# Performance work log

Hardware: AMD Instinct MI355X
Metric: run time of the kernel (lower is better)

Reference implementation:

```python
import jax, jax.numpy as jnp
import numpy as np

B, OUT, IN = 1024, 512, 1024

def setup_inputs() -> dict:
    key = jax.random.key(0)
    k1, k2, k3, k4 = jax.random.split(key, 4)
    x = jax.random.uniform(k1, (B, IN), dtype=jnp.float32)            # inputs in [0,1]
    w = jax.random.uniform(k2, (OUT, IN), dtype=jnp.float32)          # centers in [min_input, max_input]=[0,1]
    u = jax.random.uniform(k3, (OUT, IN), dtype=jnp.float32, minval=0.2, maxval=0.7)  # slopes per init
    andor01 = jax.random.randint(k4, (1, OUT), 0, 2).astype(jnp.float32)  # frozen 0/1 mix ('*' mode)
    return {"x": x, "w": w, "u": u, "andor01": andor01}

def reference(x, w, u, andor01):
    # xuw = u * (x[b,None,i] - w[o,i]) ; z[b,o] = sum_i xuw^2 ; y = exp(-z)
    diff = u[None, :, :] * (x[:, None, :] - w[None, :, :])   # [B, OUT, IN]
    z = jnp.sum(diff * diff, axis=-1)                        # [B, OUT]
    y = jnp.exp(-z)                                          # forward of LargeAttractorExp
    # andor == '*': y + andor01 * (1 - 2y)
    return y + andor01 * (1.0 - 2.0 * y)
```

## Files before the change

kernel.cpp:

```cpp
#include <hip/hip_runtime.h>

#define B_SZ   1024
#define OUT_SZ 512
#define IN_SZ  1024

#define MB 64
#define NB 64
#define KSPLIT 4
#define KSL (IN_SZ / KSPLIT)
#define CH  64
#define NCH (KSL / CH)

typedef __bf16 bf16x8 __attribute__((ext_vector_type(8)));
typedef __bf16 bf16x4 __attribute__((ext_vector_type(4)));
typedef float  f32x4  __attribute__((ext_vector_type(4)));

#define A_IDX(seg, s, mf, slot) (((((seg)*2 + (s))*4 + (mf))*64 + (slot))*8)
#define B_IDX(seg, s, nf, slot) (((((seg)*2 + (s))*4 + (nf))*64 + (slot))*8)

__global__ __launch_bounds__(256) void rbf_fused(
    const float* __restrict__ x, const float* __restrict__ w,
    const float* __restrict__ u, float* __restrict__ part)
{
    __shared__ __bf16 Asm[2 * 2 * 4 * 64 * 8];
    __shared__ __bf16 Bsm[3 * 2 * 4 * 64 * 8];

    const int t     = threadIdx.x;
    const int lane  = t & 63;
    const int wv    = t >> 6;
    const int wm    = wv >> 1;
    const int wn    = wv & 1;
    const int mBase = blockIdx.x * MB;
    const int nBase = blockIdx.y * NB;
    const int kz    = blockIdx.z;
    const int kBase = kz * KSL;

    f32x4 acc[2][2] = {};
    f32x4 acc_r[2]  = {};

    bf16x8 ones;
    #pragma unroll
    for (int j = 0; j < 8; ++j) ones[j] = (__bf16)1.f;

    float4 xr[4], ur[4], wr[4];

    auto load_regs = [&](int c) {
        #pragma unroll
        for (int i = 0; i < 4; ++i) {
            int id  = i * 256 + t;
            int row = id >> 4;
            int gk  = kBase + c * CH + (id & 15) * 4;
            xr[i] = *(const float4*)&x[(size_t)(mBase + row) * IN_SZ + gk];
            ur[i] = *(const float4*)&u[(size_t)(nBase + row) * IN_SZ + gk];
            wr[i] = *(const float4*)&w[(size_t)(nBase + row) * IN_SZ + gk];
        }
    };

    auto write_lds = [&]() {
        #pragma unroll
        for (int i = 0; i < 4; ++i) {
            int id    = i * 256 + t;
            int row   = id >> 4;
            int row16 = row & 15;
            int frag  = row >> 4;
            int kl    = (id & 15) * 4;
            int s     = kl >> 5;
            int quad  = (kl >> 3) & 3;
            int j0    = kl & 7;
            int slot  = quad * 16 + ((row16 ^ quad) & 15);

            float xv[4] = {xr[i].x, xr[i].y, xr[i].z, xr[i].w};
            float uv[4] = {ur[i].x, ur[i].y, ur[i].z, ur[i].w};
            float wv4[4] = {wr[i].x, wr[i].y, wr[i].z, wr[i].w};
            bf16x4 a0, a1, b0, b1, b2;
            #pragma unroll
            for (int e = 0; e < 4; ++e) {
                float xe = xv[e], ue = uv[e], we = wv4[e];
                float u2 = ue * ue;
                float uw = ue * we;
                a0[e] = (__bf16)(xe * xe);
                a1[e] = (__bf16)xe;
                b0[e] = (__bf16)u2;
                b1[e] = (__bf16)(-2.f * u2 * we);
                b2[e] = (__bf16)(uw * uw);
            }
            *(bf16x4*)&Asm[A_IDX(0, s, frag, slot) + j0] = a0;
            *(bf16x4*)&Asm[A_IDX(1, s, frag, slot) + j0] = a1;
            *(bf16x4*)&Bsm[B_IDX(0, s, frag, slot) + j0] = b0;
            *(bf16x4*)&Bsm[B_IDX(1, s, frag, slot) + j0] = b1;
            *(bf16x4*)&Bsm[B_IDX(2, s, frag, slot) + j0] = b2;
        }
    };

    const int r_quad = lane >> 4;
    const int r_slot = r_quad * 16 + (((lane & 15) ^ r_quad) & 15);
    const int mf0 = wm * 2, nf0 = wn * 2;

    load_regs(0);

    for (int c = 0; c < NCH; ++c) {
        __syncthreads();
        write_lds();
        __syncthreads();
        if (c + 1 < NCH) load_regs(c + 1);

        #pragma unroll
        for (int seg = 0; seg < 2; ++seg)
            #pragma unroll
            for (int s = 0; s < 2; ++s) {
                bf16x8 am0 = *(const bf16x8*)&Asm[A_IDX(seg, s, mf0,     r_slot)];
                bf16x8 am1 = *(const bf16x8*)&Asm[A_IDX(seg, s, mf0 + 1, r_slot)];
                bf16x8 bn0 = *(const bf16x8*)&Bsm[B_IDX(seg, s, nf0,     r_slot)];
                bf16x8 bn1 = *(const bf16x8*)&Bsm[B_IDX(seg, s, nf0 + 1, r_slot)];
                acc[0][0] = __builtin_amdgcn_mfma_f32_16x16x32_bf16(am0, bn0, acc[0][0], 0, 0, 0);
                acc[0][1] = __builtin_amdgcn_mfma_f32_16x16x32_bf16(am0, bn1, acc[0][1], 0, 0, 0);
                acc[1][0] = __builtin_amdgcn_mfma_f32_16x16x32_bf16(am1, bn0, acc[1][0], 0, 0, 0);
                acc[1][1] = __builtin_amdgcn_mfma_f32_16x16x32_bf16(am1, bn1, acc[1][1], 0, 0, 0);
            }
        #pragma unroll
        for (int s = 0; s < 2; ++s) {
            bf16x8 b20 = *(const bf16x8*)&Bsm[B_IDX(2, s, nf0,     r_slot)];
            bf16x8 b21 = *(const bf16x8*)&Bsm[B_IDX(2, s, nf0 + 1, r_slot)];
            acc_r[0] = __builtin_amdgcn_mfma_f32_16x16x32_bf16(ones, b20, acc_r[0], 0, 0, 0);
            acc_r[1] = __builtin_amdgcn_mfma_f32_16x16x32_bf16(ones, b21, acc_r[1], 0, 0, 0);
        }
    }

    const int col = lane & 15;
    #pragma unroll
    for (int mi = 0; mi < 2; ++mi) {
        int b = mBase + (wm * 2 + mi) * 16 + r_quad * 4;
        #pragma unroll
        for (int ni = 0; ni < 2; ++ni) {
            int o = nBase + (wn * 2 + ni) * 16 + col;
            #pragma unroll
            for (int r = 0; r < 4; ++r)
                part[((size_t)kz * B_SZ + (b + r)) * OUT_SZ + o] =
                    acc[mi][ni][r] + acc_r[ni][r];
        }
    }
}

__global__ __launch_bounds__(256) void rbf_reduce(
    const float* __restrict__ part, const float* __restrict__ andor,
    float* __restrict__ out)
{
    int idx = blockIdx.x * 256 + threadIdx.x;
    if (idx < B_SZ * OUT_SZ) {
        float z = 0.f;
        #pragma unroll
        for (int kz = 0; kz < KSPLIT; ++kz)
            z += part[(size_t)kz * (B_SZ * OUT_SZ) + idx];
        float a = andor[idx & (OUT_SZ - 1)];
        float y = __expf(-z);
        out[idx] = fmaf(y, 1.f - 2.f * a, a);
    }
}

extern "C" void kernel_launch(void* const* d_in, const int* in_sizes, int n_in,
                              void* d_out, int out_size, void* d_ws, size_t ws_size,
                              hipStream_t stream) {
    const float* x = (const float*)d_in[0];
    const float* w = (const float*)d_in[1];
    const float* u = (const float*)d_in[2];
    const float* a = (const float*)d_in[3];
    float* out = (float*)d_out;

    float* part = (float*)d_ws;

    dim3 grid(B_SZ / MB, OUT_SZ / NB, KSPLIT);
    rbf_fused<<<grid, dim3(256), 0, stream>>>(x, w, u, part);
    rbf_reduce<<<dim3((B_SZ * OUT_SZ) / 256), dim3(256), 0, stream>>>(part, a, out);
}
```

Measured before the change: 75.32 us.

## Precompute bf16 operand images in a prep kernel and stream them via global-to-LDS loads

```diff
diff --git a/kernel.cpp b/kernel.cpp
--- a/kernel.cpp
+++ b/kernel.cpp
@@ -3,158 +3,184 @@
 #define B_SZ   1024
 #define OUT_SZ 512
 #define IN_SZ  1024
+#define KK     2048
 
 #define MB 64
 #define NB 64
-#define KSPLIT 4
-#define KSL (IN_SZ / KSPLIT)
+#define KSPLIT 8
+#define KSL (KK / KSPLIT)
 #define CH  64
 #define NCH (KSL / CH)
+#define NKC (KK / CH)
+#define CHUNK_ENT 512
 
 typedef __bf16 bf16x8 __attribute__((ext_vector_type(8)));
-typedef __bf16 bf16x4 __attribute__((ext_vector_type(4)));
 typedef float  f32x4  __attribute__((ext_vector_type(4)));
 
-#define A_IDX(seg, s, mf, slot) (((((seg)*2 + (s))*4 + (mf))*64 + (slot))*8)
-#define B_IDX(seg, s, nf, slot) (((((seg)*2 + (s))*4 + (nf))*64 + (slot))*8)
-
-__global__ __launch_bounds__(256) void rbf_fused(
+#define PART_BYTES ((size_t)KSPLIT * B_SZ * OUT_SZ * 4)
+#define AIMG_OFF   PART_BYTES
+#define AIMG_BYTES ((size_t)(B_SZ / MB) * NKC * CHUNK_ENT * 16)
+#define BIMG_OFF   (AIMG_OFF + AIMG_BYTES)
+#define BIMG_BYTES ((size_t)(OUT_SZ / NB) * NKC * CHUNK_ENT * 16)
+#define RB_OFF     (BIMG_OFF + BIMG_BYTES)
+
+__global__ __launch_bounds__(256) void rbf_prep(
     const float* __restrict__ x, const float* __restrict__ w,
-    const float* __restrict__ u, float* __restrict__ part)
+    const float* __restrict__ u, __bf16* __restrict__ Aimg,
+    __bf16* __restrict__ Bimg, float* __restrict__ rbias)
 {
-    __shared__ __bf16 Asm[2 * 2 * 4 * 64 * 8];
-    __shared__ __bf16 Bsm[3 * 2 * 4 * 64 * 8];
-
-    const int t     = threadIdx.x;
-    const int lane  = t & 63;
-    const int wv    = t >> 6;
-    const int wm    = wv >> 1;
-    const int wn    = wv & 1;
-    const int mBase = blockIdx.x * MB;
-    const int nBase = blockIdx.y * NB;
-    const int kz    = blockIdx.z;
-    const int kBase = kz * KSL;
+    const int bid = blockIdx.x, t = threadIdx.x;
+    if (bid < 1024) {
+        const int e    = (bid << 8) + t;
+        const int slot = e & 63;
+        const int frag = (e >> 6) & 3;
+        const int s    = (e >> 8) & 1;
+        const int kc   = (e >> 9) & 31;
+        const int mT   = e >> 14;
+        const int row  = mT * 64 + frag * 16 + (slot & 15);
+        const int k0   = kc * 64 + s * 32 + (slot >> 4) * 8;
+        const float* src = &x[(size_t)row * IN_SZ + (k0 & (IN_SZ - 1))];
+        float4 v0 = *(const float4*)src;
+        float4 v1 = *(const float4*)(src + 4);
+        float vv[8] = {v0.x, v0.y, v0.z, v0.w, v1.x, v1.y, v1.z, v1.w};
+        bf16x8 o8;
+        if (k0 < IN_SZ) {
+            #pragma unroll
+            for (int j = 0; j < 8; ++j) o8[j] = (__bf16)(vv[j] * vv[j]);
+        } else {
+            #pragma unroll
+            for (int j = 0; j < 8; ++j) o8[j] = (__bf16)vv[j];
+        }
+        *(bf16x8*)&Aimg[(size_t)e * 8] = o8;
+    } else if (bid < 1536) {
+        const int e    = ((bid - 1024) << 8) + t;
+        const int slot = e & 63;
+        const int frag = (e >> 6) & 3;
+        const int s    = (e >> 8) & 1;
+        const int kc   = (e >> 9) & 31;
+        const int nT   = e >> 14;
+        const int row  = nT * 64 + frag * 16 + (slot & 15);
+        const int k0   = kc * 64 + s * 32 + (slot >> 4) * 8;
+        const size_t off = (size_t)row * IN_SZ + (k0 & (IN_SZ - 1));
+        float4 u0 = *(const float4*)&u[off];
+        float4 u1 = *(const float4*)&u[off + 4];
+        float uu[8] = {u0.x, u0.y, u0.z, u0.w, u1.x, u1.y, u1.z, u1.w};
+        bf16x8 o8;
+        if (k0 < IN_SZ) {
+            #pragma unroll
+            for (int j = 0; j < 8; ++j) o8[j] = (__bf16)(uu[j] * uu[j]);
+        } else {
+            float4 w0 = *(const float4*)&w[off];
+            float4 w1 = *(const float4*)&w[off + 4];
+            float ww[8] = {w0.x, w0.y, w0.z, w0.w, w1.x, w1.y, w1.z, w1.w};
+            #pragma unroll
+            for (int j = 0; j < 8; ++j) o8[j] = (__bf16)(-2.f * uu[j] * uu[j] * ww[j]);
+        }
+        *(bf16x8*)&Bimg[(size_t)e * 8] = o8;
+    } else {
+        const int o = ((bid - 1536) << 5) + (t >> 3);
+        const size_t base = (size_t)o * IN_SZ + (size_t)(t & 7) * 128;
+        float s = 0.f;
+        for (int k2 = 0; k2 < 128; k2 += 4) {
+            float4 uu = *(const float4*)&u[base + k2];
+            float4 ww = *(const float4*)&w[base + k2];
+            float p0 = uu.x * ww.x, p1 = uu.y * ww.y;
+            float p2 = uu.z * ww.z, p3 = uu.w * ww.w;
+            s = fmaf(p0, p0, s); s = fmaf(p1, p1, s);
+            s = fmaf(p2, p2, s); s = fmaf(p3, p3, s);
+        }
+        s += __shfl_xor(s, 1);
+        s += __shfl_xor(s, 2);
+        s += __shfl_xor(s, 4);
+        if ((t & 7) == 0) rbias[o] = s;
+    }
+}
+
+__device__ __forceinline__ void gld_lds16(const __bf16* g, __bf16* l) {
+    __builtin_amdgcn_global_load_lds(
+        (const __attribute__((address_space(1))) void*)g,
+        (__attribute__((address_space(3))) void*)l, 16, 0, 0);
+}
+
+__global__ __launch_bounds__(256) void rbf_gemm(
+    const __bf16* __restrict__ Aimg, const __bf16* __restrict__ Bimg,
+    float* __restrict__ part)
+{
+    __shared__ __bf16 Asm[2][CHUNK_ENT * 8];
+    __shared__ __bf16 Bsm[2][CHUNK_ENT * 8];
+
+    const int t = threadIdx.x, lane = t & 63;
+    const int wv = t >> 6, wm = wv >> 1, wn = wv & 1;
+    const int mT = blockIdx.x, nT = blockIdx.y, kz = blockIdx.z;
 
     f32x4 acc[2][2] = {};
-    f32x4 acc_r[2]  = {};
-
-    bf16x8 ones;
-    #pragma unroll
-    for (int j = 0; j < 8; ++j) ones[j] = (__bf16)1.f;
-
-    float4 xr[4], ur[4], wr[4];
-
-    auto load_regs = [&](int c) {
-        #pragma unroll
-        for (int i = 0; i < 4; ++i) {
-            int id  = i * 256 + t;
-            int row = id >> 4;
-            int gk  = kBase + c * CH + (id & 15) * 4;
-            xr[i] = *(const float4*)&x[(size_t)(mBase + row) * IN_SZ + gk];
-            ur[i] = *(const float4*)&u[(size_t)(nBase + row) * IN_SZ + gk];
-            wr[i] = *(const float4*)&w[(size_t)(nBase + row) * IN_SZ + gk];
-        }
+
+    const __bf16* gA = &Aimg[(size_t)(mT * NKC + kz * NCH) * CHUNK_ENT * 8];
+    const __bf16* gB = &Bimg[(size_t)(nT * NKC + kz * NCH) * CHUNK_ENT * 8];
+
+    auto stage = [&](int buf, int c) {
+        const __bf16* ga = gA + (size_t)c * CHUNK_ENT * 8;
+        const __bf16* gb = gB + (size_t)c * CHUNK_ENT * 8;
+        gld_lds16(ga + (size_t)t * 8,         &Asm[buf][t * 8]);
+        gld_lds16(ga + (size_t)(t + 256) * 8, &Asm[buf][(t + 256) * 8]);
+        gld_lds16(gb + (size_t)t * 8,         &Bsm[buf][t * 8]);
+        gld_lds16(gb + (size_t)(t + 256) * 8, &Bsm[buf][(t + 256) * 8]);
     };
 
-    auto write_lds = [&]() {
-        #pragma unroll
-        for (int i = 0; i < 4; ++i) {
-            int id    = i * 256 + t;
-            int row   = id >> 4;
-            int row16 = row & 15;
-            int frag  = row >> 4;
-            int kl    = (id & 15) * 4;
-            int s     = kl >> 5;
-            int quad  = (kl >> 3) & 3;
-            int j0    = kl & 7;
-            int slot  = quad * 16 + ((row16 ^ quad) & 15);
-
-            float xv[4] = {xr[i].x, xr[i].y, xr[i].z, xr[i].w};
-            float uv[4] = {ur[i].x, ur[i].y, ur[i].z, ur[i].w};
-            float wv4[4] = {wr[i].x, wr[i].y, wr[i].z, wr[i].w};
-            bf16x4 a0, a1, b0, b1, b2;
-            #pragma unroll
-            for (int e = 0; e < 4; ++e) {
-                float xe = xv[e], ue = uv[e], we = wv4[e];
-                float u2 = ue * ue;
-                float uw = ue * we;
-                a0[e] = (__bf16)(xe * xe);
-                a1[e] = (__bf16)xe;
-                b0[e] = (__bf16)u2;
-                b1[e] = (__bf16)(-2.f * u2 * we);
-                b2[e] = (__bf16)(uw * uw);
-            }
-            *(bf16x4*)&Asm[A_IDX(0, s, frag, slot) + j0] = a0;
-            *(bf16x4*)&Asm[A_IDX(1, s, frag, slot) + j0] = a1;
-            *(bf16x4*)&Bsm[B_IDX(0, s, frag, slot) + j0] = b0;
-            *(bf16x4*)&Bsm[B_IDX(1, s, frag, slot) + j0] = b1;
-            *(bf16x4*)&Bsm[B_IDX(2, s, frag, slot) + j0] = b2;
-        }
-    };
-
-    const int r_quad = lane >> 4;
-    const int r_slot = r_quad * 16 + (((lane & 15) ^ r_quad) & 15);
-    const int mf0 = wm * 2, nf0 = wn * 2;
-
-    load_regs(0);
-
+    stage(0, 0);
+    #pragma unroll
     for (int c = 0; c < NCH; ++c) {
         __syncthreads();
-        write_lds();
-        __syncthreads();
-        if (c + 1 < NCH) load_regs(c + 1);
-
-        #pragma unroll
-        for (int seg = 0; seg < 2; ++seg)
-            #pragma unroll
-            for (int s = 0; s < 2; ++s) {
-                bf16x8 am0 = *(const bf16x8*)&Asm[A_IDX(seg, s, mf0,     r_slot)];
-                bf16x8 am1 = *(const bf16x8*)&Asm[A_IDX(seg, s, mf0 + 1, r_slot)];
-                bf16x8 bn0 = *(const bf16x8*)&Bsm[B_IDX(seg, s, nf0,     r_slot)];
-                bf16x8 bn1 = *(const bf16x8*)&Bsm[B_IDX(seg, s, nf0 + 1, r_slot)];
-                acc[0][0] = __builtin_amdgcn_mfma_f32_16x16x32_bf16(am0, bn0, acc[0][0], 0, 0, 0);
-                acc[0][1] = __builtin_amdgcn_mfma_f32_16x16x32_bf16(am0, bn1, acc[0][1], 0, 0, 0);
-                acc[1][0] = __builtin_amdgcn_mfma_f32_16x16x32_bf16(am1, bn0, acc[1][0], 0, 0, 0);
-                acc[1][1] = __builtin_amdgcn_mfma_f32_16x16x32_bf16(am1, bn1, acc[1][1], 0, 0, 0);
-            }
+        if (c + 1 < NCH) stage((c + 1) & 1, c + 1);
+        const __bf16* Ab = Asm[c & 1];
+        const __bf16* Bb = Bsm[c & 1];
         #pragma unroll
         for (int s = 0; s < 2; ++s) {
-            bf16x8 b20 = *(const bf16x8*)&Bsm[B_IDX(2, s, nf0,     r_slot)];
-            bf16x8 b21 = *(const bf16x8*)&Bsm[B_IDX(2, s, nf0 + 1, r_slot)];
-            acc_r[0] = __builtin_amdgcn_mfma_f32_16x16x32_bf16(ones, b20, acc_r[0], 0, 0, 0);
-            acc_r[1] = __builtin_amdgcn_mfma_f32_16x16x32_bf16(ones, b21, acc_r[1], 0, 0, 0);
-        }
-    }
-
-    const int col = lane & 15;
+            bf16x8 a0 = *(const bf16x8*)&Ab[((s * 4 + wm * 2    ) * 64 + lane) * 8];
+            bf16x8 a1 = *(const bf16x8*)&Ab[((s * 4 + wm * 2 + 1) * 64 + lane) * 8];
+            bf16x8 b0 = *(const bf16x8*)&Bb[((s * 4 + wn * 2    ) * 64 + lane) * 8];
+            bf16x8 b1 = *(const bf16x8*)&Bb[((s * 4 + wn * 2 + 1) * 64 + lane) * 8];
+            acc[0][0] = __builtin_amdgcn_mfma_f32_16x16x32_bf16(a0, b0, acc[0][0], 0, 0, 0);
+            acc[0][1] = __builtin_amdgcn_mfma_f32_16x16x32_bf16(a0, b1, acc[0][1], 0, 0, 0);
+            acc[1][0] = __builtin_amdgcn_mfma_f32_16x16x32_bf16(a1, b0, acc[1][0], 0, 0, 0);
+            acc[1][1] = __builtin_amdgcn_mfma_f32_16x16x32_bf16(a1, b1, acc[1][1], 0, 0, 0);
+        }
+    }
+
+    const int col = lane & 15, rq = lane >> 4;
     #pragma unroll
     for (int mi = 0; mi < 2; ++mi) {
-        int b = mBase + (wm * 2 + mi) * 16 + r_quad * 4;
+        const int b = mT * MB + (wm * 2 + mi) * 16 + rq * 4;
         #pragma unroll
         for (int ni = 0; ni < 2; ++ni) {
-            int o = nBase + (wn * 2 + ni) * 16 + col;
+            const int o = nT * NB + (wn * 2 + ni) * 16 + col;
             #pragma unroll
             for (int r = 0; r < 4; ++r)
-                part[((size_t)kz * B_SZ + (b + r)) * OUT_SZ + o] =
-                    acc[mi][ni][r] + acc_r[ni][r];
+                part[((size_t)kz * B_SZ + (b + r)) * OUT_SZ + o] = acc[mi][ni][r];
         }
     }
 }
 
 __global__ __launch_bounds__(256) void rbf_reduce(
-    const float* __restrict__ part, const float* __restrict__ andor,
-    float* __restrict__ out)
+    const float* __restrict__ part, const float* __restrict__ rbias,
+    const float* __restrict__ andor, float* __restrict__ out)
 {
-    int idx = blockIdx.x * 256 + threadIdx.x;
-    if (idx < B_SZ * OUT_SZ) {
-        float z = 0.f;
-        #pragma unroll
-        for (int kz = 0; kz < KSPLIT; ++kz)
-            z += part[(size_t)kz * (B_SZ * OUT_SZ) + idx];
-        float a = andor[idx & (OUT_SZ - 1)];
-        float y = __expf(-z);
-        out[idx] = fmaf(y, 1.f - 2.f * a, a);
-    }
+    const int i4   = blockIdx.x * 256 + threadIdx.x;
+    const int base = i4 * 4;
+    f32x4 z = {};
+    #pragma unroll
+    for (int kz = 0; kz < KSPLIT; ++kz)
+        z += *(const f32x4*)&part[(size_t)kz * (B_SZ * OUT_SZ) + base];
+    const int o = base & (OUT_SZ - 1);
+    f32x4 rb = *(const f32x4*)&rbias[o];
+    f32x4 av = *(const f32x4*)&andor[o];
+    f32x4 res;
+    #pragma unroll
+    for (int j = 0; j < 4; ++j) {
+        float y = __expf(-(z[j] + rb[j]));
+        res[j] = fmaf(y, 1.f - 2.f * av[j], av[j]);
+    }
+    *(f32x4*)&out[base] = res;
 }
 
 extern "C" void kernel_launch(void* const* d_in, const int* in_sizes, int n_in,
@@ -166,9 +192,12 @@
     const float* a = (const float*)d_in[3];
     float* out = (float*)d_out;
 
-    float* part = (float*)d_ws;
-
-    dim3 grid(B_SZ / MB, OUT_SZ / NB, KSPLIT);
-    rbf_fused<<<grid, dim3(256), 0, stream>>>(x, w, u, part);
-    rbf_reduce<<<dim3((B_SZ * OUT_SZ) / 256), dim3(256), 0, stream>>>(part, a, out);
-}
+    float*  part  = (float*)d_ws;
+    __bf16* Aimg  = (__bf16*)((char*)d_ws + AIMG_OFF);
+    __bf16* Bimg  = (__bf16*)((char*)d_ws + BIMG_OFF);
+    float*  rbias = (float*)((char*)d_ws + RB_OFF);
+
+    rbf_prep  <<<dim3(1552),      dim3(256), 0, stream>>>(x, w, u, Aimg, Bimg, rbias);
+    rbf_gemm  <<<dim3(16, 8, 8),  dim3(256), 0, stream>>>(Aimg, Bimg, part);
+    rbf_reduce<<<dim3(512),       dim3(256), 0, stream>>>(part, rbias, a, out);
+}
```

Result: slower. 84.28 us (+11.9%).

## Fuse split-K partials and reduction into one single-pass RBF kernel

Applied to the files above, without the earlier changes.

```diff
diff --git a/kernel.cpp b/kernel.cpp
--- a/kernel.cpp
+++ b/kernel.cpp
@@ -5,155 +5,127 @@
 #define IN_SZ  1024
 
 #define MB 64
-#define NB 64
-#define KSPLIT 4
-#define KSL (IN_SZ / KSPLIT)
-#define CH  64
-#define NCH (KSL / CH)
+#define NB 32
+#define NKC 16
 
 typedef __bf16 bf16x8 __attribute__((ext_vector_type(8)));
 typedef __bf16 bf16x4 __attribute__((ext_vector_type(4)));
 typedef float  f32x4  __attribute__((ext_vector_type(4)));
 
 #define A_IDX(seg, s, mf, slot) (((((seg)*2 + (s))*4 + (mf))*64 + (slot))*8)
-#define B_IDX(seg, s, nf, slot) (((((seg)*2 + (s))*4 + (nf))*64 + (slot))*8)
+#define B_IDX(seg, s, nf, slot) (((((seg)*2 + (s))*2 + (nf))*64 + (slot))*8)
 
-__global__ __launch_bounds__(256) void rbf_fused(
+__global__ __launch_bounds__(512) void rbf_one(
     const float* __restrict__ x, const float* __restrict__ w,
-    const float* __restrict__ u, float* __restrict__ part)
+    const float* __restrict__ u, const float* __restrict__ andor,
+    float* __restrict__ out)
 {
     __shared__ __bf16 Asm[2 * 2 * 4 * 64 * 8];
-    __shared__ __bf16 Bsm[3 * 2 * 4 * 64 * 8];
+    __shared__ __bf16 Bsm[2 * 2 * 2 * 64 * 8];
+    __shared__ float  r_lds[NB];
 
-    const int t     = threadIdx.x;
-    const int lane  = t & 63;
-    const int wv    = t >> 6;
-    const int wm    = wv >> 1;
-    const int wn    = wv & 1;
-    const int mBase = blockIdx.x * MB;
-    const int nBase = blockIdx.y * NB;
-    const int kz    = blockIdx.z;
-    const int kBase = kz * KSL;
+    const int t    = threadIdx.x;
+    const int lane = t & 63;
+    const int wv   = t >> 6;
+    const int wm   = wv >> 1;
+    const int wn   = wv & 1;
 
-    f32x4 acc[2][2] = {};
-    f32x4 acc_r[2]  = {};
+    const int bid = blockIdx.x;
+    const int swz = (bid & 7) * 32 + (bid >> 3);
+    const int mT = swz & 15, nT = swz >> 4;
+    const int mBase = mT * MB, nBase = nT * NB;
 
-    bf16x8 ones;
-    #pragma unroll
-    for (int j = 0; j < 8; ++j) ones[j] = (__bf16)1.f;
+    f32x4 acc = {};
+    float rp = 0.f;
 
-    float4 xr[4], ur[4], wr[4];
+    const int arow = t >> 4;
+    const int akl  = (t & 15) * 4;
+    const int brow = t >> 4;
 
+    float4 xr[2], ur, wr;
     auto load_regs = [&](int c) {
-        #pragma unroll
-        for (int i = 0; i < 4; ++i) {
-            int id  = i * 256 + t;
-            int row = id >> 4;
-            int gk  = kBase + c * CH + (id & 15) * 4;
-            xr[i] = *(const float4*)&x[(size_t)(mBase + row) * IN_SZ + gk];
-            ur[i] = *(const float4*)&u[(size_t)(nBase + row) * IN_SZ + gk];
-            wr[i] = *(const float4*)&w[(size_t)(nBase + row) * IN_SZ + gk];
-        }
+        const int gk = c * 64 + akl;
+        xr[0] = *(const float4*)&x[(size_t)(mBase + arow)      * IN_SZ + gk];
+        xr[1] = *(const float4*)&x[(size_t)(mBase + 32 + arow) * IN_SZ + gk];
+        ur    = *(const float4*)&u[(size_t)(nBase + brow)      * IN_SZ + gk];
+        wr    = *(const float4*)&w[(size_t)(nBase + brow)      * IN_SZ + gk];
     };
+
+    const int sW   = akl >> 5;
+    const int quad = (akl >> 3) & 3;
+    const int j0   = akl & 7;
 
     auto write_lds = [&]() {
         #pragma unroll
-        for (int i = 0; i < 4; ++i) {
-            int id    = i * 256 + t;
-            int row   = id >> 4;
-            int row16 = row & 15;
-            int frag  = row >> 4;
-            int kl    = (id & 15) * 4;
-            int s     = kl >> 5;
-            int quad  = (kl >> 3) & 3;
-            int j0    = kl & 7;
-            int slot  = quad * 16 + ((row16 ^ quad) & 15);
-
-            float xv[4] = {xr[i].x, xr[i].y, xr[i].z, xr[i].w};
-            float uv[4] = {ur[i].x, ur[i].y, ur[i].z, ur[i].w};
-            float wv4[4] = {wr[i].x, wr[i].y, wr[i].z, wr[i].w};
-            bf16x4 a0, a1, b0, b1, b2;
+        for (int i = 0; i < 2; ++i) {
+            const int row   = i * 32 + arow;
+            const int frag  = row >> 4;
+            const int slot  = quad * 16 + (((row & 15) ^ quad) & 15);
+            float v[4] = {xr[i].x, xr[i].y, xr[i].z, xr[i].w};
+            bf16x4 a0, a1;
             #pragma unroll
             for (int e = 0; e < 4; ++e) {
-                float xe = xv[e], ue = uv[e], we = wv4[e];
-                float u2 = ue * ue;
-                float uw = ue * we;
-                a0[e] = (__bf16)(xe * xe);
-                a1[e] = (__bf16)xe;
+                a0[e] = (__bf16)(v[e] * v[e]);
+                a1[e] = (__bf16)v[e];
+            }
+            *(bf16x4*)&Asm[A_IDX(0, sW, frag, slot) + j0] = a0;
+            *(bf16x4*)&Asm[A_IDX(1, sW, frag, slot) + j0] = a1;
+        }
+        {
+            const int frag = brow >> 4;
+            const int slot = quad * 16 + (((brow & 15) ^ quad) & 15);
+            float uv[4] = {ur.x, ur.y, ur.z, ur.w};
+            float wv4[4] = {wr.x, wr.y, wr.z, wr.w};
+            bf16x4 b0, b1;
+            #pragma unroll
+            for (int e = 0; e < 4; ++e) {
+                float u2 = uv[e] * uv[e];
+                float p  = uv[e] * wv4[e];
                 b0[e] = (__bf16)u2;
-                b1[e] = (__bf16)(-2.f * u2 * we);
-                b2[e] = (__bf16)(uw * uw);
+                b1[e] = (__bf16)(-2.f * u2 * wv4[e]);
+                rp = fmaf(p, p, rp);
             }
-            *(bf16x4*)&Asm[A_IDX(0, s, frag, slot) + j0] = a0;
-            *(bf16x4*)&Asm[A_IDX(1, s, frag, slot) + j0] = a1;
-            *(bf16x4*)&Bsm[B_IDX(0, s, frag, slot) + j0] = b0;
-            *(bf16x4*)&Bsm[B_IDX(1, s, frag, slot) + j0] = b1;
-            *(bf16x4*)&Bsm[B_IDX(2, s, frag, slot) + j0] = b2;
+            *(bf16x4*)&Bsm[B_IDX(0, sW, frag, slot) + j0] = b0;
+            *(bf16x4*)&Bsm[B_IDX(1, sW, frag, slot) + j0] = b1;
         }
     };
 
     const int r_quad = lane >> 4;
     const int r_slot = r_quad * 16 + (((lane & 15) ^ r_quad) & 15);
-    const int mf0 = wm * 2, nf0 = wn * 2;
 
     load_regs(0);
-
-    for (int c = 0; c < NCH; ++c) {
+    for (int c = 0; c < NKC; ++c) {
         __syncthreads();
         write_lds();
         __syncthreads();
-        if (c + 1 < NCH) load_regs(c + 1);
-
+        if (c + 1 < NKC) load_regs(c + 1);
         #pragma unroll
         for (int seg = 0; seg < 2; ++seg)
             #pragma unroll
-            for (int s = 0; s < 2; ++s) {
-                bf16x8 am0 = *(const bf16x8*)&Asm[A_IDX(seg, s, mf0,     r_slot)];
-                bf16x8 am1 = *(const bf16x8*)&Asm[A_IDX(seg, s, mf0 + 1, r_slot)];
-                bf16x8 bn0 = *(const bf16x8*)&Bsm[B_IDX(seg, s, nf0,     r_slot)];
-                bf16x8 bn1 = *(const bf16x8*)&Bsm[B_IDX(seg, s, nf0 + 1, r_slot)];
-                acc[0][0] = __builtin_amdgcn_mfma_f32_16x16x32_bf16(am0, bn0, acc[0][0], 0, 0, 0);
-                acc[0][1] = __builtin_amdgcn_mfma_f32_16x16x32_bf16(am0, bn1, acc[0][1], 0, 0, 0);
-                acc[1][0] = __builtin_amdgcn_mfma_f32_16x16x32_bf16(am1, bn0, acc[1][0], 0, 0, 0);
-                acc[1][1] = __builtin_amdgcn_mfma_f32_16x16x32_bf16(am1, bn1, acc[1][1], 0, 0, 0);
+            for (int s2 = 0; s2 < 2; ++s2) {
+                bf16x8 am = *(const bf16x8*)&Asm[A_IDX(seg, s2, wm, r_slot)];
+                bf16x8 bn = *(const bf16x8*)&Bsm[B_IDX(seg, s2, wn, r_slot)];
+                acc = __builtin_amdgcn_mfma_f32_16x16x32_bf16(am, bn, acc, 0, 0, 0);
             }
-        #pragma unroll
-        for (int s = 0; s < 2; ++s) {
-            bf16x8 b20 = *(const bf16x8*)&Bsm[B_IDX(2, s, nf0,     r_slot)];
-            bf16x8 b21 = *(const bf16x8*)&Bsm[B_IDX(2, s, nf0 + 1, r_slot)];
-            acc_r[0] = __builtin_amdgcn_mfma_f32_16x16x32_bf16(ones, b20, acc_r[0], 0, 0, 0);
-            acc_r[1] = __builtin_amdgcn_mfma_f32_16x16x32_bf16(ones, b21, acc_r[1], 0, 0, 0);
-        }
     }
 
-    const int col = lane & 15;
+    rp += __shfl_xor(rp, 1);
+    rp += __shfl_xor(rp, 2);
+    rp += __shfl_xor(rp, 4);
+    rp += __shfl_xor(rp, 8);
+    if ((lane & 15) == 0) r_lds[brow] = rp;
+    __syncthreads();
+
+    const int col = lane & 15, rq = lane >> 4;
+    const int b = mBase + wm * 16 + rq * 4;
+    const int o = nBase + wn * 16 + col;
+    const float rv = r_lds[wn * 16 + col];
+    const float a  = andor[o];
+    const float cf = 1.f - 2.f * a;
     #pragma unroll
-    for (int mi = 0; mi < 2; ++mi) {
-        int b = mBase + (wm * 2 + mi) * 16 + r_quad * 4;
-        #pragma unroll
-        for (int ni = 0; ni < 2; ++ni) {
-            int o = nBase + (wn * 2 + ni) * 16 + col;
-            #pragma unroll
-            for (int r = 0; r < 4; ++r)
-                part[((size_t)kz * B_SZ + (b + r)) * OUT_SZ + o] =
-                    acc[mi][ni][r] + acc_r[ni][r];
-        }
-    }
-}
-
-__global__ __launch_bounds__(256) void rbf_reduce(
-    const float* __restrict__ part, const float* __restrict__ andor,
-    float* __restrict__ out)
-{
-    int idx = blockIdx.x * 256 + threadIdx.x;
-    if (idx < B_SZ * OUT_SZ) {
-        float z = 0.f;
-        #pragma unroll
-        for (int kz = 0; kz < KSPLIT; ++kz)
-            z += part[(size_t)kz * (B_SZ * OUT_SZ) + idx];
-        float a = andor[idx & (OUT_SZ - 1)];
-        float y = __expf(-z);
-        out[idx] = fmaf(y, 1.f - 2.f * a, a);
+    for (int r = 0; r < 4; ++r) {
+        float y = __expf(-(acc[r] + rv));
+        out[(size_t)(b + r) * OUT_SZ + o] = fmaf(y, cf, a);
     }
 }
 
@@ -166,9 +138,6 @@
     const float* a = (const float*)d_in[3];
     float* out = (float*)d_out;
 
-    float* part = (float*)d_ws;
-
-    dim3 grid(B_SZ / MB, OUT_SZ / NB, KSPLIT);
-    rbf_fused<<<grid, dim3(256), 0, stream>>>(x, w, u, part);
-    rbf_reduce<<<dim3((B_SZ * OUT_SZ) / 256), dim3(256), 0, stream>>>(part, a, out);
+    rbf_one<<<dim3((B_SZ / MB) * (OUT_SZ / NB)), dim3(512), 0, stream>>>(
+        x, w, u, a, out);
 }
```

Result: no change. 75.87 us (+0.7%).
